# Performance work log

Hardware: AMD Instinct MI355X
Metric: run time of the kernel (lower is better)

The kernel has to match this reference:

```python
import jax, jax.numpy as jnp
import numpy as np
from jax import lax

IDC = 8          # in_dim_caps
ROUTINGS = 3
BN_EPS = 1e-5


def squash(s, axis=-1):
    mag_sq = jnp.sum(s * s, axis=axis, keepdims=True)
    mag = jnp.sqrt(mag_sq)
    return mag_sq / (1.0 + mag_sq) * (s / (mag + 1e-8))


def setup_inputs() -> dict:
    key = jax.random.key(0)
    ks = jax.random.split(key, 8)
    B, P, S = 64, 512, 8
    O, OD, Z = 32, 16, 64
    I = S * S * (P // IDC)  # 4096 input capsules
    return {
        "x": jax.random.normal(ks[0], (B, P, S, S), jnp.float32),
        "conv_w": 0.02 * jax.random.normal(ks[1], (P, P, 3, 3), jnp.float32),
        "bn_gamma": jnp.ones((P,), jnp.float32),
        "bn_beta": jnp.zeros((P,), jnp.float32),
        "bn_mean": jnp.zeros((P,), jnp.float32),
        "bn_var": jnp.ones((P,), jnp.float32),
        "caps_w": 0.01 * jax.random.normal(ks[2], (O, I, OD, IDC), jnp.float32),
        "fcm_w1": 0.02 * jax.random.normal(ks[3], (OD, 1024), jnp.float32),
        "fcm_b1": jnp.zeros((1024,), jnp.float32),
        "fcm_w2": 0.02 * jax.random.normal(ks[4], (1024, Z), jnp.float32),
        "fcm_b2": jnp.zeros((Z,), jnp.float32),
        "fcv_w": 0.02 * jax.random.normal(ks[5], (OD, Z), jnp.float32),
        "fcv_b": jnp.zeros((Z,), jnp.float32),
    }


def reference(x, conv_w, bn_gamma, bn_beta, bn_mean, bn_var, caps_w,
              fcm_w1, fcm_b1, fcm_w2, fcm_b2, fcv_w, fcv_b):
    # conv_pose: Conv3x3 (no bias) -> BatchNorm (eval, running stats) -> ReLU
    y = lax.conv_general_dilated(x, conv_w, (1, 1), 'SAME',
                                 dimension_numbers=('NCHW', 'OIHW', 'NCHW'))
    inv = bn_gamma / jnp.sqrt(bn_var + BN_EPS)
    y = (y - bn_mean[None, :, None, None]) * inv[None, :, None, None] + bn_beta[None, :, None, None]
    y = jax.nn.relu(y)

    B, P, S, _ = y.shape
    # [B, P//IDC, IDC, S, S] -> [B, P//IDC, S, S, IDC] -> [B, I, IDC]
    pose = y.reshape(B, P // IDC, IDC, S, S).transpose(0, 1, 3, 4, 2).reshape(B, -1, IDC)
    pose = squash(pose)

    # x_hat[b,o,i,d] = sum_k W[o,i,d,k] * pose[b,i,k]
    x_hat = jnp.einsum('oidk,bik->boid', caps_w, pose)
    x_hat_d = lax.stop_gradient(x_hat)

    b = jnp.zeros(x_hat.shape[:3], x_hat.dtype)  # [B, O, I]
    out = None
    for i in range(ROUTINGS):
        c = jax.nn.softmax(b, axis=1)  # softmax over output capsules
        if i == ROUTINGS - 1:
            out = squash(jnp.einsum('boi,boid->bod', c, x_hat))
        else:
            v = squash(jnp.einsum('boi,boid->bod', c, x_hat_d))
            b = b + jnp.einsum('bod,boid->boi', v, x_hat_d)

    # VAE head (eval mode: z = z_mu)
    h = jax.nn.relu(out @ fcm_w1 + fcm_b1)
    z_mu = h @ fcm_w2 + fcm_b2
    z_var = jax.nn.softplus(out @ fcv_w + fcv_b) + 1e-8
    z = z_mu
    return (z, z_mu, z_var)
```

## Files before the change

kernel.cpp:

```cpp
#include <hip/hip_runtime.h>
#include <cstdint>
#include <cstddef>

#define B 64
#define PCH 512
#define O_CAPS 32
#define OD 16
#define IDC 8
#define I_CAPS 4096
#define ICHUNK 16
#define NPBLK 256
#define KDIM 4608

typedef __attribute__((ext_vector_type(8))) short bf16x8;
typedef __attribute__((ext_vector_type(4))) float f32x4;
typedef __attribute__((ext_vector_type(8))) unsigned short u16x8;
typedef _Float16 h2 __attribute__((ext_vector_type(2)));
typedef _Float16 f16x8v __attribute__((ext_vector_type(8)));

#if defined(__has_builtin)
#if __has_builtin(__builtin_amdgcn_fdot2)
#define HAVE_FDOT2 1
#endif
#endif

#define OFF_PH 0
#define SZ_PH (B * I_CAPS * IDC / 2)
#define OFF_PART (OFF_PH + SZ_PH)
#define SZ_PART ((size_t)NPBLK * 4 * 16 * 512)
#define OFF_AIM OFF_PART
#define OFF_PV0 OFF_PART
#define OFF_SPILL (OFF_PART + SZ_PART)
#define OFF_VBUF (OFF_SPILL + 1048576)
#define SZ_V (B * O_CAPS * OD)
#define OFF_VBUF2 (OFF_VBUF + SZ_V)
#define OFF_OUTC (OFF_VBUF2 + SZ_V)
#define OFF_WB (OFF_OUTC + SZ_V)
#define OFF_BIAS (OFF_WB + (PCH * KDIM) / 2)
#define OFF_WRH (OFF_BIAS + 512)
#define SZ_WRH ((size_t)O_CAPS * I_CAPS * OD * IDC / 2)

__device__ inline unsigned short f2bf(float f) {
  union { float f; unsigned int u; } v; v.f = f;
  unsigned int r = v.u + 0x7fff + ((v.u >> 16) & 1);
  return (unsigned short)(r >> 16);
}

union HU { u16x8 v; _Float16 h[8]; h2 p[4]; };

__device__ inline unsigned short f2h(float f) {
  union { _Float16 h; unsigned short u; } c;
  c.h = (_Float16)f;
  return c.u;
}

__global__ __launch_bounds__(256) void cast_f16x8(
    const float* __restrict__ src, unsigned short* __restrict__ dst) {
  const size_t t = (size_t)blockIdx.x * 256 + threadIdx.x;
  const float4* s = (const float4*)src + t * 2;
  const float4 a = s[0], b = s[1];
  HU u;
  u.h[0] = (_Float16)a.x; u.h[1] = (_Float16)a.y;
  u.h[2] = (_Float16)a.z; u.h[3] = (_Float16)a.w;
  u.h[4] = (_Float16)b.x; u.h[5] = (_Float16)b.y;
  u.h[6] = (_Float16)b.z; u.h[7] = (_Float16)b.w;
  ((u16x8*)dst)[t] = u.v;
}

__global__ __launch_bounds__(256) void prep_wb(
    const float* __restrict__ cw, const float* __restrict__ gamma,
    const float* __restrict__ beta, const float* __restrict__ mean,
    const float* __restrict__ var, unsigned short* __restrict__ wb,
    float* __restrict__ bias) {
  const int n = blockIdx.x;
  const float inv = gamma[n] * rsqrtf(var[n] + 1e-5f);
  if (threadIdx.x == 0) bias[n] = beta[n] - mean[n] * inv;
  for (int k = threadIdx.x; k < KDIM; k += 256)
    wb[(size_t)n * KDIM + k] = f2bf(cw[(size_t)n * KDIM + k] * inv);
}

__global__ __launch_bounds__(256) void prep_aim(
    const float* __restrict__ x, unsigned short* __restrict__ aim) {
  __shared__ float lxp[32 * 100];
  const int b = blockIdx.x;
  const int ci0 = blockIdx.y * 32;
  const int tid = threadIdx.x;
  for (int t = tid; t < 3200; t += 256) lxp[t] = 0.f;
  __syncthreads();
  for (int t = tid; t < 2048; t += 256) {
    const int ci = t >> 6, px = t & 63;
    lxp[ci * 100 + 11 + (px >> 3) * 10 + (px & 7)] =
        x[((size_t)b * PCH + ci0 + ci) * 64 + px];
  }
  __syncthreads();
  for (int t = tid; t < 4608; t += 256) {
    const int px = t / 72;
    const int kk = (t - px * 72) * 4;
    unsigned short v[4];
#pragma unroll
    for (int j = 0; j < 4; ++j) {
      const int k = kk + j;
      const int ci = k / 9;
      const int tap = k - ci * 9;
      const int kh = tap / 3, kw = tap - kh * 3;
      v[j] = f2bf(lxp[ci * 100 + ((px >> 3) + kh) * 10 + (px & 7) + kw]);
    }
    ushort4* dst =
        (ushort4*)(aim + (size_t)(b * 64 + px) * KDIM + ci0 * 9 + kk);
    *dst = make_ushort4(v[0], v[1], v[2], v[3]);
  }
}

__global__ __launch_bounds__(256) void conv_gemm(
    const unsigned short* __restrict__ aim, const unsigned short* __restrict__ wb,
    const float* __restrict__ bias, unsigned short* __restrict__ pose_h) {
  __shared__ unsigned short lA[64 * 64];
  __shared__ unsigned short lB[64 * 64];
  const int tid = threadIdx.x;
  const int lane = tid & 63, wv = tid >> 6;
  const int wm = wv & 1, wn = wv >> 1;
  const int m0 = blockIdx.x * 64;
  const int n0 = blockIdx.y * 64;
  const int rsub = lane >> 3, seg = lane & 7;

  f32x4 acc[2][2];
#pragma unroll
  for (int a = 0; a < 2; ++a)
#pragma unroll
    for (int c = 0; c < 2; ++c) acc[a][c] = (f32x4){0.f, 0.f, 0.f, 0.f};

  for (int k0 = 0; k0 < KDIM; k0 += 64) {
    __syncthreads();
#pragma unroll
    for (int it = 0; it < 2; ++it) {
      const int r = it * 32 + wv * 8 + rsub;
      const int c = seg ^ (r & 7);
      const unsigned short* ga = aim + (size_t)(m0 + r) * KDIM + k0 + c * 8;
      __builtin_amdgcn_global_load_lds(
          (const __attribute__((address_space(1))) void*)ga,
          (__attribute__((address_space(3))) void*)(lA + (it * 32 + wv * 8) * 64),
          16, 0, 0);
      const unsigned short* gb = wb + (size_t)(n0 + r) * KDIM + k0 + c * 8;
      __builtin_amdgcn_global_load_lds(
          (const __attribute__((address_space(1))) void*)gb,
          (__attribute__((address_space(3))) void*)(lB + (it * 32 + wv * 8) * 64),
          16, 0, 0);
    }
    __syncthreads();
#pragma unroll
    for (int kc = 0; kc < 2; ++kc) {
      const int g = kc * 4 + (lane >> 4);
      const int ml = wm * 32 + (lane & 15);
      const int nl = wn * 32 + (lane & 15);
      const int sa = (g ^ (ml & 7)) * 8;
      const int sb = (g ^ (nl & 7)) * 8;
      const bf16x8 a0 = *(const bf16x8*)(lA + (ml + 0) * 64 + sa);
      const bf16x8 a1 = *(const bf16x8*)(lA + (ml + 16) * 64 + sa);
      const bf16x8 b0 = *(const bf16x8*)(lB + (nl + 0) * 64 + sb);
      const bf16x8 b1 = *(const bf16x8*)(lB + (nl + 16) * 64 + sb);
      acc[0][0] = __builtin_amdgcn_mfma_f32_16x16x32_bf16(a0, b0, acc[0][0], 0, 0, 0);
      acc[0][1] = __builtin_amdgcn_mfma_f32_16x16x32_bf16(a0, b1, acc[0][1], 0, 0, 0);
      acc[1][0] = __builtin_amdgcn_mfma_f32_16x16x32_bf16(a1, b0, acc[1][0], 0, 0, 0);
      acc[1][1] = __builtin_amdgcn_mfma_f32_16x16x32_bf16(a1, b1, acc[1][1], 0, 0, 0);
    }
  }

  const int bq = blockIdx.x;
  float bsv[2];
#pragma unroll
  for (int ni = 0; ni < 2; ++ni)
    bsv[ni] = bias[n0 + wn * 32 + ni * 16 + (lane & 15)];
#pragma unroll
  for (int mi = 0; mi < 2; ++mi) {
#pragma unroll
    for (int ni = 0; ni < 2; ++ni) {
      const int n = n0 + wn * 32 + ni * 16 + (lane & 15);
#pragma unroll
      for (int reg = 0; reg < 4; ++reg) {
        float v = fmaxf(acc[mi][ni][reg] + bsv[ni], 0.f);
        float s2 = v * v;
        s2 += __shfl_xor(s2, 1, 64);
        s2 += __shfl_xor(s2, 2, 64);
        s2 += __shfl_xor(s2, 4, 64);
        const float sc = s2 / (1.f + s2) / (sqrtf(s2) + 1e-8f);
        const int px = wm * 32 + mi * 16 + (lane >> 4) * 4 + reg;
        pose_h[((size_t)bq * I_CAPS + (n >> 3) * 64 + px) * IDC + (n & 7)] =
            f2h(v * sc);
      }
    }
  }
}

__global__ __launch_bounds__(256) void caps_v0(
    const unsigned short* __restrict__ pose_h,
    const unsigned short* __restrict__ wrh, float* __restrict__ pv0) {
  __shared__ unsigned short lA[64 * 64];
  __shared__ unsigned short lB[64 * 64];
  const int tid = threadIdx.x;
  const int lane = tid & 63, wv = tid >> 6;
  const int wm = wv & 1, wn = wv >> 1;
  const int o0 = blockIdx.x * 4;
  const int ks = blockIdx.y;
  const int rsub = lane >> 3, seg = lane & 7;

  f32x4 acc[2][2];
#pragma unroll
  for (int a = 0; a < 2; ++a)
#pragma unroll
    for (int c = 0; c < 2; ++c) acc[a][c] = (f32x4){0.f, 0.f, 0.f, 0.f};

  for (int kt = 0; kt < 16; ++kt) {
    const int k0 = ks * 1024 + kt * 64;
    const int i0 = k0 >> 3;
    __syncthreads();
#pragma unroll
    for (int it = 0; it < 2; ++it) {
      const int r = it * 32 + wv * 8 + rsub;
      const int c = seg ^ (r & 7);
      const unsigned short* ga = pose_h + (size_t)r * 32768 + k0 + c * 8;
      __builtin_amdgcn_global_load_lds(
          (const __attribute__((address_space(1))) void*)ga,
          (__attribute__((address_space(3))) void*)(lA + (it * 32 + wv * 8) * 64),
          16, 0, 0);
    }
#pragma unroll
    for (int h = 0; h < 2; ++h) {
      const int idx = h * 256 + tid;
      const int d = idx & 15;
      const int il = (idx >> 4) & 7;
      const int ol = idx >> 7;
      const u16x8 v = *(const u16x8*)(wrh + (size_t)(o0 + ol) * 524288 +
                                      (size_t)(i0 + il) * 128 + d * 8);
      const int np = ol * 16 + d;
      *(u16x8*)(lB + np * 64 + (il ^ (np & 7)) * 8) = v;
    }
    __syncthreads();
#pragma unroll
    for (int kc = 0; kc < 2; ++kc) {
      const int g = kc * 4 + (lane >> 4);
      const int ml = wm * 32 + (lane & 15);
      const int nl = wn * 32 + (lane & 15);
      const int sa = (g ^ (ml & 7)) * 8;
      const int sb = (g ^ (nl & 7)) * 8;
      const f16x8v a0 = *(const f16x8v*)(lA + (ml + 0) * 64 + sa);
      const f16x8v a1 = *(const f16x8v*)(lA + (ml + 16) * 64 + sa);
      const f16x8v b0 = *(const f16x8v*)(lB + (nl + 0) * 64 + sb);
      const f16x8v b1 = *(const f16x8v*)(lB + (nl + 16) * 64 + sb);
      acc[0][0] = __builtin_amdgcn_mfma_f32_16x16x32_f16(a0, b0, acc[0][0], 0, 0, 0);
      acc[0][1] = __builtin_amdgcn_mfma_f32_16x16x32_f16(a0, b1, acc[0][1], 0, 0, 0);
      acc[1][0] = __builtin_amdgcn_mfma_f32_16x16x32_f16(a1, b0, acc[1][0], 0, 0, 0);
      acc[1][1] = __builtin_amdgcn_mfma_f32_16x16x32_f16(a1, b1, acc[1][1], 0, 0, 0);
    }
  }
#pragma unroll
  for (int mi = 0; mi < 2; ++mi) {
#pragma unroll
    for (int ni = 0; ni < 2; ++ni) {
      const int n = blockIdx.x * 64 + wn * 32 + ni * 16 + (lane & 15);
#pragma unroll
      for (int reg = 0; reg < 4; ++reg) {
        const int m = wm * 32 + mi * 16 + (lane >> 4) * 4 + reg;
        pv0[(size_t)(ks * 64 + m) * 512 + n] = acc[mi][ni][reg];
      }
    }
  }
}

__global__ __launch_bounds__(256) void reduce_v0(
    const float* __restrict__ pv0, float* __restrict__ vbuf) {
  const int t = blockIdx.x * 256 + threadIdx.x;
  const int b = t >> 9;
  const int r = t & 511;
  float s = 0.f;
#pragma unroll 8
  for (int ks = 0; ks < 32; ++ks)
    s += pv0[(size_t)(ks * 64 + b) * 512 + r];
  s *= (1.0f / 32.0f);
  float sq = s * s;
  sq += __shfl_xor(sq, 1, 64);
  sq += __shfl_xor(sq, 2, 64);
  sq += __shfl_xor(sq, 4, 64);
  sq += __shfl_xor(sq, 8, 64);
  const float sc = sq / (1.f + sq) / (sqrtf(sq) + 1e-8f);
  vbuf[t] = s * sc;
}

__global__ __launch_bounds__(256, 2) void routing_phase(
    const unsigned short* __restrict__ pose_h,
    const unsigned short* __restrict__ wrh,
    const float* __restrict__ vb, float* __restrict__ partials) {
  __shared__ u16x8 lw[2][8 * 65];
  const int tid = threadIdx.x;
  const int lane = tid & 63;
  const int wv = tid >> 6;
  const int o = lane >> 1, dh = lane & 1;
  const int i0 = blockIdx.x * ICHUNK;
  const int b0 = blockIdx.y * 16;

  const int sl = tid >> 3;
  const int sq = tid & 7;
  const u16x8* wr8 = (const u16x8*)wrh;

  float acc[4][8];
  float vr[4][8];
#pragma unroll
  for (int bb = 0; bb < 4; ++bb) {
    const int b = b0 + wv * 4 + bb;
    const float4* vp =
        (const float4*)(vb + ((size_t)(b * O_CAPS + o) * OD) + dh * 8);
    const float4 v0 = vp[0], v1 = vp[1];
    vr[bb][0] = v0.x; vr[bb][1] = v0.y; vr[bb][2] = v0.z; vr[bb][3] = v0.w;
    vr[bb][4] = v1.x; vr[bb][5] = v1.y; vr[bb][6] = v1.z; vr[bb][7] = v1.w;
#pragma unroll
    for (int j = 0; j < 8; ++j) acc[bb][j] = 0.f;
  }

  auto stage = [&](int i, int buf) {
#pragma unroll
    for (int half = 0; half < 2; ++half) {
      const int l = sl + half * 32;
      lw[buf][sq * 65 + l] =
          wr8[(size_t)(l >> 1) * (I_CAPS * 16) + (size_t)i * 16 +
              (l & 1) * 8 + sq];
    }
  };

  stage(i0, 0);
  __syncthreads();

  for (int ii = 0; ii < ICHUNK; ++ii) {
    const int buf = ii & 1;
    if (ii + 1 < ICHUNK) stage(i0 + ii + 1, buf ^ 1);
    const int i = i0 + ii;
    HU w[8];
#pragma unroll
    for (int q = 0; q < 8; ++q) w[q].v = lw[buf][q * 65 + lane];
#pragma unroll
    for (int bb = 0; bb < 4; ++bb) {
      const int b = b0 + wv * 4 + bb;
      HU pk;
      pk.v = *(const u16x8*)(pose_h + ((size_t)b * I_CAPS + i) * IDC);
      float X[8];
#pragma unroll
      for (int j = 0; j < 8; ++j) {
#ifdef HAVE_FDOT2
        float s = __builtin_amdgcn_fdot2(w[j].p[3], pk.p[3], 0.f, false);
        s = __builtin_amdgcn_fdot2(w[j].p[2], pk.p[2], s, false);
        s = __builtin_amdgcn_fdot2(w[j].p[1], pk.p[1], s, false);
        X[j] = __builtin_amdgcn_fdot2(w[j].p[0], pk.p[0], s, false);
#else
        float s = 0.f;
#pragma unroll
        for (int k = 0; k < 8; ++k) s += (float)w[j].h[k] * (float)pk.h[k];
        X[j] = s;
#endif
      }
      float lg = 0.f;
#pragma unroll
      for (int j = 0; j < 8; ++j) lg += vr[bb][j] * X[j];
      lg += __shfl_xor(lg, 1, 64);
      const float e = __expf(lg);
      float sm = e;
#pragma unroll
      for (int s = 2; s < 64; s <<= 1) sm += __shfl_xor(sm, s, 64);
      const float c = e / sm;
#pragma unroll
      for (int j = 0; j < 8; ++j) acc[bb][j] += c * X[j];
    }
    __syncthreads();
  }

  const size_t pbase = ((size_t)blockIdx.x * 4 + blockIdx.y) * (16 * 512);
#pragma unroll
  for (int bb = 0; bb < 4; ++bb) {
    const int bl = wv * 4 + bb;
    float4* dst =
        (float4*)(partials + pbase + (size_t)bl * 512 + o * 16 + dh * 8);
    dst[0] = make_float4(acc[bb][0], acc[bb][1], acc[bb][2], acc[bb][3]);
    dst[1] = make_float4(acc[bb][4], acc[bb][5], acc[bb][6], acc[bb][7]);
  }
}

template <int ADDV>
__global__ __launch_bounds__(256) void reduce_squash(
    const float* __restrict__ partials, const float* __restrict__ vprev,
    float* __restrict__ dst) {
  const int t = blockIdx.x * 256 + threadIdx.x;
  const int b = t >> 9;
  const int r = t & 511;
  const int bg = b >> 4, bl = b & 15;
  const size_t elem = (size_t)bl * 512 + r;
  float s = 0.f;
  for (int blk = 0; blk < NPBLK; ++blk)
    s += partials[(size_t)(blk * 4 + bg) * (16 * 512) + elem];
  float sq = s * s;
  sq += __shfl_xor(sq, 1, 64);
  sq += __shfl_xor(sq, 2, 64);
  sq += __shfl_xor(sq, 4, 64);
  sq += __shfl_xor(sq, 8, 64);
  const float sc = sq / (1.f + sq) / (sqrtf(sq) + 1e-8f);
  float val = s * sc;
  if (ADDV) val += vprev[t];
  dst[t] = val;
}

__global__ __launch_bounds__(1024) void vae_head(
    const float* __restrict__ outc, const float* __restrict__ w1,
    const float* __restrict__ b1, const float* __restrict__ w2,
    const float* __restrict__ b2, const float* __restrict__ wv,
    const float* __restrict__ bv, float* __restrict__ dout) {
  __shared__ float lo[4][16];
  __shared__ float lh[4][1024];
  __shared__ float red[16][4][64];
  const int n0 = blockIdx.x * 4;
  const int tid = threadIdx.x;
  if (tid < 64) lo[tid >> 4][tid & 15] = outc[(size_t)n0 * 16 + tid];
  __syncthreads();

  {
    const float bb = b1[tid];
    float h0 = bb, h1 = bb, h2v = bb, h3 = bb;
#pragma unroll
    for (int k = 0; k < 16; ++k) {
      const float w = w1[(size_t)k * 1024 + tid];
      h0 += lo[0][k] * w;
      h1 += lo[1][k] * w;
      h2v += lo[2][k] * w;
      h3 += lo[3][k] * w;
    }
    lh[0][tid] = fmaxf(h0, 0.f);
    lh[1][tid] = fmaxf(h1, 0.f);
    lh[2][tid] = fmaxf(h2v, 0.f);
    lh[3][tid] = fmaxf(h3, 0.f);
  }
  __syncthreads();

  const int m = tid & 63, sl = tid >> 6;
  {
    float a0 = 0.f, a1 = 0.f, a2 = 0.f, a3 = 0.f;
    const int j0 = sl * 64;
#pragma unroll 4
    for (int jj = 0; jj < 64; ++jj) {
      const int j = j0 + jj;
      const float w = w2[(size_t)j * 64 + m];
      a0 += lh[0][j] * w;
      a1 += lh[1][j] * w;
      a2 += lh[2][j] * w;
      a3 += lh[3][j] * w;
    }
    red[sl][0][m] = a0;
    red[sl][1][m] = a1;
    red[sl][2][m] = a2;
    red[sl][3][m] = a3;
  }
  __syncthreads();

  if (tid < 256) {
    const int r = tid >> 6;
    float z = b2[m];
#pragma unroll
    for (int s = 0; s < 16; ++s) z += red[s][r][m];
    const int n = n0 + r;
    dout[n * 64 + m] = z;
    dout[131072 + n * 64 + m] = z;
    float sv = bv[m];
#pragma unroll
    for (int k = 0; k < 16; ++k) sv += lo[r][k] * wv[(size_t)k * 64 + m];
    const float sp =
        (sv > 0.f) ? (sv + log1pf(__expf(-sv))) : log1pf(__expf(sv));
    dout[262144 + n * 64 + m] = sp + 1e-8f;
  }
}

extern "C" void kernel_launch(void* const* d_in, const int* in_sizes, int n_in,
                              void* d_out, int out_size, void* d_ws,
                              size_t ws_size, hipStream_t stream) {
  const float* x = (const float*)d_in[0];
  const float* conv_w = (const float*)d_in[1];
  const float* bn_gamma = (const float*)d_in[2];
  const float* bn_beta = (const float*)d_in[3];
  const float* bn_mean = (const float*)d_in[4];
  const float* bn_var = (const float*)d_in[5];
  const float* caps_w = (const float*)d_in[6];
  const float* fcm_w1 = (const float*)d_in[7];
  const float* fcm_b1 = (const float*)d_in[8];
  const float* fcm_w2 = (const float*)d_in[9];
  const float* fcm_b2 = (const float*)d_in[10];
  const float* fcv_w = (const float*)d_in[11];
  const float* fcv_b = (const float*)d_in[12];
  float* out = (float*)d_out;
  float* ws = (float*)d_ws;

  unsigned short* pose_h = (unsigned short*)(ws + OFF_PH);
  float* part = ws + OFF_PART;
  float* pv0 = ws + OFF_PV0;
  float* vbuf = ws + OFF_VBUF;
  float* vbuf2 = ws + OFF_VBUF2;
  float* outc = ws + OFF_OUTC;
  unsigned short* wbq = (unsigned short*)(ws + OFF_WB);
  float* bias = ws + OFF_BIAS;
  unsigned short* wrh = (unsigned short*)(ws + OFF_WRH);
  unsigned short* aim = (unsigned short*)(ws + OFF_AIM);

  cast_f16x8<<<8192, 256, 0, stream>>>(caps_w, wrh);
  prep_wb<<<512, 256, 0, stream>>>(conv_w, bn_gamma, bn_beta, bn_mean, bn_var,
                                   wbq, bias);
  prep_aim<<<dim3(64, 16), 256, 0, stream>>>(x, aim);
  conv_gemm<<<dim3(64, 8), 256, 0, stream>>>(aim, wbq, bias, pose_h);

  caps_v0<<<dim3(8, 32), 256, 0, stream>>>(pose_h, wrh, pv0);
  reduce_v0<<<128, 256, 0, stream>>>(pv0, vbuf);

  routing_phase<<<dim3(NPBLK, 4), 256, 0, stream>>>(pose_h, wrh, vbuf, part);
  reduce_squash<1><<<128, 256, 0, stream>>>(part, vbuf, vbuf2);

  routing_phase<<<dim3(NPBLK, 4), 256, 0, stream>>>(pose_h, wrh, vbuf2, part);
  reduce_squash<0><<<128, 256, 0, stream>>>(part, nullptr, outc);

  vae_head<<<512, 1024, 0, stream>>>(outc, fcm_w1, fcm_b1, fcm_w2, fcm_b2,
                                     fcv_w, fcv_b, out);
}
```

Baseline: 367.4 us.

## Split routing into MFMA logits/softmax kernel and coupling-weighted MFMA GEMM

Replaces the fused scalar routing_phase (fdot2 per capsule, in-register softmax, accumulation) with two kernels. logits_softmax computes W·v with MFMA, contracts it with pose to get the logits, applies softmax over output capsules, and writes the coupling coefficients to a buffer in fp16. out_gemm reuses the caps_v0 GEMM structure and scales the A fragments by those coefficients before each MFMA. The aim is to move the dominant routing arithmetic onto matrix cores. In exchange it adds a coefficient buffer round-trip through memory, extra launches, and fp16 rounding of the coefficients.

```diff
diff --git a/kernel.cpp b/kernel.cpp
--- a/kernel.cpp
+++ b/kernel.cpp
@@ -8,8 +8,6 @@
 #define OD 16
 #define IDC 8
 #define I_CAPS 4096
-#define ICHUNK 16
-#define NPBLK 256
 #define KDIM 4608
 
 typedef __attribute__((ext_vector_type(8))) short bf16x8;
@@ -18,18 +16,13 @@
 typedef _Float16 h2 __attribute__((ext_vector_type(2)));
 typedef _Float16 f16x8v __attribute__((ext_vector_type(8)));
 
-#if defined(__has_builtin)
-#if __has_builtin(__builtin_amdgcn_fdot2)
-#define HAVE_FDOT2 1
-#endif
-#endif
-
 #define OFF_PH 0
 #define SZ_PH (B * I_CAPS * IDC / 2)
 #define OFF_PART (OFF_PH + SZ_PH)
-#define SZ_PART ((size_t)NPBLK * 4 * 16 * 512)
+#define SZ_PART ((size_t)256 * 4 * 16 * 512)
 #define OFF_AIM OFF_PART
-#define OFF_PV0 OFF_PART
+#define OFF_PV OFF_PART
+#define OFF_CH (OFF_PART + 1048576)
 #define OFF_SPILL (OFF_PART + SZ_PART)
 #define OFF_VBUF (OFF_SPILL + 1048576)
 #define SZ_V (B * O_CAPS * OD)
@@ -46,12 +39,18 @@
   return (unsigned short)(r >> 16);
 }
 
-union HU { u16x8 v; _Float16 h[8]; h2 p[4]; };
+union HU { u16x8 v; f16x8v f; _Float16 h[8]; h2 p[4]; };
 
 __device__ inline unsigned short f2h(float f) {
   union { _Float16 h; unsigned short u; } c;
   c.h = (_Float16)f;
   return c.u;
+}
+
+__device__ inline float h2f(unsigned short u) {
+  union { unsigned short u; _Float16 h; } c;
+  c.u = u;
+  return (float)c.h;
 }
 
 __global__ __launch_bounds__(256) void cast_f16x8(
@@ -193,7 +192,7 @@
 
 __global__ __launch_bounds__(256) void caps_v0(
     const unsigned short* __restrict__ pose_h,
-    const unsigned short* __restrict__ wrh, float* __restrict__ pv0) {
+    const unsigned short* __restrict__ wrh, float* __restrict__ pv) {
   __shared__ unsigned short lA[64 * 64];
   __shared__ unsigned short lB[64 * 64];
   const int tid = threadIdx.x;
@@ -260,139 +259,196 @@
 #pragma unroll
       for (int reg = 0; reg < 4; ++reg) {
         const int m = wm * 32 + mi * 16 + (lane >> 4) * 4 + reg;
-        pv0[(size_t)(ks * 64 + m) * 512 + n] = acc[mi][ni][reg];
+        pv[(size_t)(ks * 64 + m) * 512 + n] = acc[mi][ni][reg];
       }
     }
   }
 }
 
-__global__ __launch_bounds__(256) void reduce_v0(
-    const float* __restrict__ pv0, float* __restrict__ vbuf) {
+__global__ __launch_bounds__(256) void out_gemm(
+    const unsigned short* __restrict__ pose_h,
+    const unsigned short* __restrict__ wrh,
+    const unsigned short* __restrict__ ch, float* __restrict__ pv) {
+  __shared__ unsigned short lA[64 * 64];
+  __shared__ unsigned short lB[64 * 64];
+  __shared__ unsigned short clds[4 * 64 * 8];
+  const int tid = threadIdx.x;
+  const int lane = tid & 63, wv = tid >> 6;
+  const int wm = wv & 1, wn = wv >> 1;
+  const int o0 = blockIdx.x * 4;
+  const int ks = blockIdx.y;
+  const int rsub = lane >> 3, seg = lane & 7;
+  const _Float16* chl = (const _Float16*)clds;
+
+  f32x4 acc[2][2];
+#pragma unroll
+  for (int a = 0; a < 2; ++a)
+#pragma unroll
+    for (int c = 0; c < 2; ++c) acc[a][c] = (f32x4){0.f, 0.f, 0.f, 0.f};
+
+  for (int kt = 0; kt < 16; ++kt) {
+    const int k0 = ks * 1024 + kt * 64;
+    const int i0 = k0 >> 3;
+    __syncthreads();
+#pragma unroll
+    for (int it = 0; it < 2; ++it) {
+      const int r = it * 32 + wv * 8 + rsub;
+      const int c = seg ^ (r & 7);
+      const unsigned short* ga = pose_h + (size_t)r * 32768 + k0 + c * 8;
+      __builtin_amdgcn_global_load_lds(
+          (const __attribute__((address_space(1))) void*)ga,
+          (__attribute__((address_space(3))) void*)(lA + (it * 32 + wv * 8) * 64),
+          16, 0, 0);
+    }
+#pragma unroll
+    for (int h = 0; h < 2; ++h) {
+      const int idx = h * 256 + tid;
+      const int d = idx & 15;
+      const int il = (idx >> 4) & 7;
+      const int ol = idx >> 7;
+      const u16x8 v = *(const u16x8*)(wrh + (size_t)(o0 + ol) * 524288 +
+                                      (size_t)(i0 + il) * 128 + d * 8);
+      const int np = ol * 16 + d;
+      *(u16x8*)(lB + np * 64 + (il ^ (np & 7)) * 8) = v;
+    }
+    {
+      const int o_l = tid >> 6, cb = tid & 63;
+      const uint4 cv = *(const uint4*)(ch + (size_t)(o0 + o_l) * (B * I_CAPS) +
+                                       (size_t)cb * I_CAPS + i0);
+      *(uint4*)&clds[(o_l * 64 + cb) * 8] = cv;
+    }
+    __syncthreads();
+#pragma unroll
+    for (int kc = 0; kc < 2; ++kc) {
+      const int g = kc * 4 + (lane >> 4);
+      const int ml = wm * 32 + (lane & 15);
+      const int nl = wn * 32 + (lane & 15);
+      const int sa = (g ^ (ml & 7)) * 8;
+      const int sb = (g ^ (nl & 7)) * 8;
+      const f16x8v a0 = *(const f16x8v*)(lA + (ml + 0) * 64 + sa);
+      const f16x8v a1 = *(const f16x8v*)(lA + (ml + 16) * 64 + sa);
+      const f16x8v b0 = *(const f16x8v*)(lB + (nl + 0) * 64 + sb);
+      const f16x8v b1 = *(const f16x8v*)(lB + (nl + 16) * 64 + sb);
+      const int ol0 = wn * 2, ol1 = wn * 2 + 1;
+      const _Float16 c00 = chl[(ol0 * 64 + ml) * 8 + g];
+      const _Float16 c01 = chl[(ol1 * 64 + ml) * 8 + g];
+      const _Float16 c10 = chl[(ol0 * 64 + ml + 16) * 8 + g];
+      const _Float16 c11 = chl[(ol1 * 64 + ml + 16) * 8 + g];
+      acc[0][0] = __builtin_amdgcn_mfma_f32_16x16x32_f16(a0 * c00, b0, acc[0][0], 0, 0, 0);
+      acc[0][1] = __builtin_amdgcn_mfma_f32_16x16x32_f16(a0 * c01, b1, acc[0][1], 0, 0, 0);
+      acc[1][0] = __builtin_amdgcn_mfma_f32_16x16x32_f16(a1 * c10, b0, acc[1][0], 0, 0, 0);
+      acc[1][1] = __builtin_amdgcn_mfma_f32_16x16x32_f16(a1 * c11, b1, acc[1][1], 0, 0, 0);
+    }
+  }
+#pragma unroll
+  for (int mi = 0; mi < 2; ++mi) {
+#pragma unroll
+    for (int ni = 0; ni < 2; ++ni) {
+      const int n = blockIdx.x * 64 + wn * 32 + ni * 16 + (lane & 15);
+#pragma unroll
+      for (int reg = 0; reg < 4; ++reg) {
+        const int m = wm * 32 + mi * 16 + (lane >> 4) * 4 + reg;
+        pv[(size_t)(ks * 64 + m) * 512 + n] = acc[mi][ni][reg];
+      }
+    }
+  }
+}
+
+__global__ __launch_bounds__(256) void logits_softmax(
+    const unsigned short* __restrict__ pose_h,
+    const unsigned short* __restrict__ wrh,
+    const float* __restrict__ vb, unsigned short* __restrict__ ch) {
+  __shared__ unsigned short ppose[16 * 132];
+  __shared__ float lgl[32 * 272];
+  const int tid = threadIdx.x;
+  const int lane = tid & 63, wv = tid >> 6;
+  const int i0 = blockIdx.x * 16;
+  const int b0 = blockIdx.y * 16;
+  const _Float16* wh = (const _Float16*)wrh;
+
+  {
+    const int b = tid >> 4, i = tid & 15;
+    const ushort4* src =
+        (const ushort4*)(pose_h + ((size_t)(b0 + b) * I_CAPS + (i0 + i)) * IDC);
+    const ushort4 p0 = src[0], p1 = src[1];
+    *(ushort4*)&ppose[b * 132 + i * 8] = p0;
+    *(ushort4*)&ppose[b * 132 + i * 8 + 4] = p1;
+  }
+  __syncthreads();
+
+  const int m = lane & 15;
+  const int g = lane >> 4;
+  const int a_isub = m >> 3, a_kk = m & 7;
+  const int c_isub = g >> 1, c_kk0 = (g & 1) * 4;
+
+  for (int o = 0; o < 32; ++o) {
+    HU bu;
+    bu.v = (u16x8){0, 0, 0, 0, 0, 0, 0, 0};
+    if (g < 2) {
+      const float4* vp =
+          (const float4*)(vb + ((size_t)(b0 + m) * O_CAPS + o) * OD + g * 8);
+      const float4 v0 = vp[0], v1 = vp[1];
+      bu.h[0] = (_Float16)v0.x; bu.h[1] = (_Float16)v0.y;
+      bu.h[2] = (_Float16)v0.z; bu.h[3] = (_Float16)v0.w;
+      bu.h[4] = (_Float16)v1.x; bu.h[5] = (_Float16)v1.y;
+      bu.h[6] = (_Float16)v1.z; bu.h[7] = (_Float16)v1.w;
+    }
+#pragma unroll
+    for (int q = 0; q < 2; ++q) {
+      const int ip = wv * 2 + q;
+      HU au;
+      au.v = (u16x8){0, 0, 0, 0, 0, 0, 0, 0};
+      if (g < 2) {
+        const int ii = i0 + ip * 2 + a_isub;
+        const size_t base =
+            (((size_t)o * I_CAPS + ii) * OD + g * 8) * IDC + a_kk;
+#pragma unroll
+        for (int j = 0; j < 8; ++j) au.h[j] = wh[base + (size_t)j * IDC];
+      }
+      const f32x4 C = __builtin_amdgcn_mfma_f32_16x16x32_f16(
+          au.f, bu.f, (f32x4){0.f, 0.f, 0.f, 0.f}, 0, 0, 0);
+      const ushort4 pk =
+          *(const ushort4*)&ppose[m * 132 + (ip * 2 + c_isub) * 8 + c_kk0];
+      float tmp = C[0] * h2f(pk.x) + C[1] * h2f(pk.y) + C[2] * h2f(pk.z) +
+                  C[3] * h2f(pk.w);
+      tmp += __shfl_xor(tmp, 16, 64);
+      if ((lane & 16) == 0) {
+        const int iw = ip * 2 + (lane >> 5);
+        lgl[o * 272 + iw * 17 + m] = tmp;
+      }
+    }
+  }
+  __syncthreads();
+
+  {
+    const int i = tid & 15, b = tid >> 4;
+    float e[32];
+    float sm = 0.f;
+#pragma unroll
+    for (int o = 0; o < 32; ++o) {
+      e[o] = __expf(lgl[o * 272 + i * 17 + b]);
+      sm += e[o];
+    }
+    const float r = 1.f / sm;
+#pragma unroll
+    for (int o = 0; o < 32; ++o)
+      ch[(size_t)o * ((size_t)B * I_CAPS) + (size_t)(b0 + b) * I_CAPS +
+         (i0 + i)] = f2h(e[o] * r);
+  }
+}
+
+template <int SCALE32, int ADDV>
+__global__ __launch_bounds__(256) void reduce_pv(
+    const float* __restrict__ pv, const float* __restrict__ vprev,
+    float* __restrict__ dst) {
   const int t = blockIdx.x * 256 + threadIdx.x;
   const int b = t >> 9;
   const int r = t & 511;
   float s = 0.f;
 #pragma unroll 8
   for (int ks = 0; ks < 32; ++ks)
-    s += pv0[(size_t)(ks * 64 + b) * 512 + r];
-  s *= (1.0f / 32.0f);
-  float sq = s * s;
-  sq += __shfl_xor(sq, 1, 64);
-  sq += __shfl_xor(sq, 2, 64);
-  sq += __shfl_xor(sq, 4, 64);
-  sq += __shfl_xor(sq, 8, 64);
-  const float sc = sq / (1.f + sq) / (sqrtf(sq) + 1e-8f);
-  vbuf[t] = s * sc;
-}
-
-__global__ __launch_bounds__(256, 2) void routing_phase(
-    const unsigned short* __restrict__ pose_h,
-    const unsigned short* __restrict__ wrh,
-    const float* __restrict__ vb, float* __restrict__ partials) {
-  __shared__ u16x8 lw[2][8 * 65];
-  const int tid = threadIdx.x;
-  const int lane = tid & 63;
-  const int wv = tid >> 6;
-  const int o = lane >> 1, dh = lane & 1;
-  const int i0 = blockIdx.x * ICHUNK;
-  const int b0 = blockIdx.y * 16;
-
-  const int sl = tid >> 3;
-  const int sq = tid & 7;
-  const u16x8* wr8 = (const u16x8*)wrh;
-
-  float acc[4][8];
-  float vr[4][8];
-#pragma unroll
-  for (int bb = 0; bb < 4; ++bb) {
-    const int b = b0 + wv * 4 + bb;
-    const float4* vp =
-        (const float4*)(vb + ((size_t)(b * O_CAPS + o) * OD) + dh * 8);
-    const float4 v0 = vp[0], v1 = vp[1];
-    vr[bb][0] = v0.x; vr[bb][1] = v0.y; vr[bb][2] = v0.z; vr[bb][3] = v0.w;
-    vr[bb][4] = v1.x; vr[bb][5] = v1.y; vr[bb][6] = v1.z; vr[bb][7] = v1.w;
-#pragma unroll
-    for (int j = 0; j < 8; ++j) acc[bb][j] = 0.f;
-  }
-
-  auto stage = [&](int i, int buf) {
-#pragma unroll
-    for (int half = 0; half < 2; ++half) {
-      const int l = sl + half * 32;
-      lw[buf][sq * 65 + l] =
-          wr8[(size_t)(l >> 1) * (I_CAPS * 16) + (size_t)i * 16 +
-              (l & 1) * 8 + sq];
-    }
-  };
-
-  stage(i0, 0);
-  __syncthreads();
-
-  for (int ii = 0; ii < ICHUNK; ++ii) {
-    const int buf = ii & 1;
-    if (ii + 1 < ICHUNK) stage(i0 + ii + 1, buf ^ 1);
-    const int i = i0 + ii;
-    HU w[8];
-#pragma unroll
-    for (int q = 0; q < 8; ++q) w[q].v = lw[buf][q * 65 + lane];
-#pragma unroll
-    for (int bb = 0; bb < 4; ++bb) {
-      const int b = b0 + wv * 4 + bb;
-      HU pk;
-      pk.v = *(const u16x8*)(pose_h + ((size_t)b * I_CAPS + i) * IDC);
-      float X[8];
-#pragma unroll
-      for (int j = 0; j < 8; ++j) {
-#ifdef HAVE_FDOT2
-        float s = __builtin_amdgcn_fdot2(w[j].p[3], pk.p[3], 0.f, false);
-        s = __builtin_amdgcn_fdot2(w[j].p[2], pk.p[2], s, false);
-        s = __builtin_amdgcn_fdot2(w[j].p[1], pk.p[1], s, false);
-        X[j] = __builtin_amdgcn_fdot2(w[j].p[0], pk.p[0], s, false);
-#else
-        float s = 0.f;
-#pragma unroll
-        for (int k = 0; k < 8; ++k) s += (float)w[j].h[k] * (float)pk.h[k];
-        X[j] = s;
-#endif
-      }
-      float lg = 0.f;
-#pragma unroll
-      for (int j = 0; j < 8; ++j) lg += vr[bb][j] * X[j];
-      lg += __shfl_xor(lg, 1, 64);
-      const float e = __expf(lg);
-      float sm = e;
-#pragma unroll
-      for (int s = 2; s < 64; s <<= 1) sm += __shfl_xor(sm, s, 64);
-      const float c = e / sm;
-#pragma unroll
-      for (int j = 0; j < 8; ++j) acc[bb][j] += c * X[j];
-    }
-    __syncthreads();
-  }
-
-  const size_t pbase = ((size_t)blockIdx.x * 4 + blockIdx.y) * (16 * 512);
-#pragma unroll
-  for (int bb = 0; bb < 4; ++bb) {
-    const int bl = wv * 4 + bb;
-    float4* dst =
-        (float4*)(partials + pbase + (size_t)bl * 512 + o * 16 + dh * 8);
-    dst[0] = make_float4(acc[bb][0], acc[bb][1], acc[bb][2], acc[bb][3]);
-    dst[1] = make_float4(acc[bb][4], acc[bb][5], acc[bb][6], acc[bb][7]);
-  }
-}
-
-template <int ADDV>
-__global__ __launch_bounds__(256) void reduce_squash(
-    const float* __restrict__ partials, const float* __restrict__ vprev,
-    float* __restrict__ dst) {
-  const int t = blockIdx.x * 256 + threadIdx.x;
-  const int b = t >> 9;
-  const int r = t & 511;
-  const int bg = b >> 4, bl = b & 15;
-  const size_t elem = (size_t)bl * 512 + r;
-  float s = 0.f;
-  for (int blk = 0; blk < NPBLK; ++blk)
-    s += partials[(size_t)(blk * 4 + bg) * (16 * 512) + elem];
+    s += pv[(size_t)(ks * 64 + b) * 512 + r];
+  if (SCALE32) s *= (1.0f / 32.0f);
   float sq = s * s;
   sq += __shfl_xor(sq, 1, 64);
   sq += __shfl_xor(sq, 2, 64);
@@ -492,8 +548,8 @@
   float* ws = (float*)d_ws;
 
   unsigned short* pose_h = (unsigned short*)(ws + OFF_PH);
-  float* part = ws + OFF_PART;
-  float* pv0 = ws + OFF_PV0;
+  float* pv = ws + OFF_PV;
+  unsigned short* ch = (unsigned short*)(ws + OFF_CH);
   float* vbuf = ws + OFF_VBUF;
   float* vbuf2 = ws + OFF_VBUF2;
   float* outc = ws + OFF_OUTC;
@@ -508,14 +564,16 @@
   prep_aim<<<dim3(64, 16), 256, 0, stream>>>(x, aim);
   conv_gemm<<<dim3(64, 8), 256, 0, stream>>>(aim, wbq, bias, pose_h);
 
-  caps_v0<<<dim3(8, 32), 256, 0, stream>>>(pose_h, wrh, pv0);
-  reduce_v0<<<128, 256, 0, stream>>>(pv0, vbuf);
-
-  routing_phase<<<dim3(NPBLK, 4), 256, 0, stream>>>(pose_h, wrh, vbuf, part);
-  reduce_squash<1><<<128, 256, 0, stream>>>(part, vbuf, vbuf2);
-
-  routing_phase<<<dim3(NPBLK, 4), 256, 0, stream>>>(pose_h, wrh, vbuf2, part);
-  reduce_squash<0><<<128, 256, 0, stream>>>(part, nullptr, outc);
+  caps_v0<<<dim3(8, 32), 256, 0, stream>>>(pose_h, wrh, pv);
+  reduce_pv<1, 0><<<128, 256, 0, stream>>>(pv, nullptr, vbuf);
+
+  logits_softmax<<<dim3(256, 4), 256, 0, stream>>>(pose_h, wrh, vbuf, ch);
+  out_gemm<<<dim3(8, 32), 256, 0, stream>>>(pose_h, wrh, ch, pv);
+  reduce_pv<0, 1><<<128, 256, 0, stream>>>(pv, vbuf, vbuf2);
+
+  logits_softmax<<<dim3(256, 4), 256, 0, stream>>>(pose_h, wrh, vbuf2, ch);
+  out_gemm<<<dim3(8, 32), 256, 0, stream>>>(pose_h, wrh, ch, pv);
+  reduce_pv<0, 0><<<128, 256, 0, stream>>>(pv, nullptr, outc);
 
   vae_head<<<512, 1024, 0, stream>>>(outc, fcm_w1, fcm_b1, fcm_w2, fcm_b2,
                                      fcv_w, fcv_b, out);
```

Result: slower. 380.8 us (+3.7%).
